# Optimization experiments

Hardware: AMD Instinct MI355X
Metric: run time of the kernel (lower is better)

The kernel has to match this reference:

```python
import jax, jax.numpy as jnp
import numpy as np
from jax import lax

K = 8  # number of KNN neighbors (excluding self)


def setup_inputs() -> dict:
    key = jax.random.key(0)
    k1, k2, k3 = jax.random.split(key, 3)
    B, H, W, C = 32, 14, 14, 2048
    OUT = 512
    x = jax.random.normal(k1, (B, H, W, C), dtype=jnp.float32)
    W1 = jax.random.normal(k2, (C, OUT), dtype=jnp.float32) * (1.0 / np.sqrt(C))
    b1 = jnp.zeros((OUT,), dtype=jnp.float32)
    W2 = jax.random.normal(k3, (OUT, OUT), dtype=jnp.float32) * (1.0 / np.sqrt(OUT))
    b2 = jnp.zeros((OUT,), dtype=jnp.float32)
    return {"x": x, "W1": W1, "b1": b1, "W2": W2, "b2": b2}


def _knn_edges(xf, k):
    # full pairwise squared-euclidean distance (monotone in cdist p=2)
    sq = jnp.sum(xf * xf, axis=-1)                      # [N]
    d2 = sq[:, None] + sq[None, :] - 2.0 * (xf @ xf.T)  # [N, N]
    _, idx = lax.top_k(-d2, k + 1)                      # smallest k+1
    knn = idx[:, 1:]                                    # drop self
    N = xf.shape[0]
    src = jnp.repeat(jnp.arange(N), k)
    dst = knn.reshape(-1)
    # GCNConv adds self-loops
    loops = jnp.arange(N)
    src = jnp.concatenate([src, loops])
    dst = jnp.concatenate([dst, loops])
    return src, dst


def _gcn_conv(h, W, b, src, dst, N):
    # PyG GCNConv: sym-normalized aggregation with self-loops
    deg = jax.ops.segment_sum(jnp.ones_like(dst, dtype=h.dtype), dst, num_segments=N)
    dinv = lax.rsqrt(jnp.maximum(deg, 1.0))
    norm = dinv[src] * dinv[dst]                        # [E]
    hw = h @ W                                          # [N, F]
    msg = hw[src] * norm[:, None]                       # gather + scale
    out = jax.ops.segment_sum(msg, dst, num_segments=N) # scatter-add
    return out + b


def reference(x, W1, b1, W2, b2):
    B, H, Wd, C = x.shape
    N = B * H * Wd
    xf = x.reshape(N, C)
    src, dst = _knn_edges(xf, K)
    h = jax.nn.relu(_gcn_conv(xf, W1, b1, src, dst, N))
    # dropout is identity in eval mode
    h = jax.nn.relu(_gcn_conv(h, W2, b2, src, dst, N))
    return h.reshape(B, H, Wd, W2.shape[1])
```

## Files before the change

### kernel.cpp

```cpp
#include <hip/hip_runtime.h>

typedef __attribute__((ext_vector_type(8))) _Float16 half8;
typedef __attribute__((ext_vector_type(4))) _Float16 half4;
typedef __attribute__((ext_vector_type(4))) float f32x4;

#define N_NODES 6272
#define CDIM    2048
#define ODIM    512
#define NPAN    49
#define NSLOT   392
#define GRID_G  1232
#define GATE    0.6f

#define XHI_OFF    0ul
#define CANDV_OFF  25690112ul
#define CANDI_OFF  35524608ul
#define SQ_OFF     40441856ul
#define KNN_OFF    40466944ul
#define DEG_OFF    41470464ul
#define DINV_OFF   41520640ul
#define RPTR_OFF   41545728ul
#define COL_OFF    41571072ul
#define W1T_OFF    41796864ul
#define W2T_OFF    43894016ul
#define HW_OFF     CANDV_OFF
#define H1H_OFF    44418304ul

__device__ __forceinline__ void gld_lds16(const void* g, void* l) {
    __builtin_amdgcn_global_load_lds(
        (const __attribute__((address_space(1))) void*)g,
        (__attribute__((address_space(3))) void*)l, 16, 0, 0);
}

__device__ __forceinline__ half8 frag_read(const char* base, int row, int s, int lane) {
    int b = (s * 4 + (lane >> 4)) ^ (row & 7);
    return *(const half8*)(base + row * 128 + b * 16);
}

#define MF(a, b, c) __builtin_amdgcn_mfma_f32_16x16x32_f16(a, b, c, 0, 0, 0)

__global__ __launch_bounds__(256) void prep_kernel(const float* __restrict__ x,
        _Float16* __restrict__ xhi, float* __restrict__ sq,
        const float* __restrict__ W1, _Float16* __restrict__ w1t,
        const float* __restrict__ W2, _Float16* __restrict__ w2t) {
    __shared__ float tile[64][65];
    int bid = blockIdx.x, tid = threadIdx.x;
    if (bid < 1568) {
        int i = bid * 4 + (tid >> 6);
        int t = tid & 63;
        const float* row = x + (size_t)i * CDIM;
        _Float16* hrow = xhi + (size_t)i * CDIM;
        float s = 0.f;
#pragma unroll
        for (int k = 0; k < 8; k++) {
            float4 v = *(const float4*)(row + (k * 64 + t) * 4);
            half4 h;
            h[0] = (_Float16)v.x; h[1] = (_Float16)v.y;
            h[2] = (_Float16)v.z; h[3] = (_Float16)v.w;
            *(half4*)(hrow + (k * 64 + t) * 4) = h;
            s += v.x * v.x + v.y * v.y + v.z * v.z + v.w * v.w;
        }
#pragma unroll
        for (int off = 32; off; off >>= 1) s += __shfl_down(s, off, 64);
        if (t == 0) sq[i] = s;
        return;
    }
    const float* W; _Float16* Wt; int K, N, idx;
    if (bid < 1824) { idx = bid - 1568; W = W1; Wt = w1t; K = CDIM; N = ODIM; }
    else            { idx = bid - 1824; W = W2; Wt = w2t; K = ODIM; N = ODIM; }
    int nkb = K / 64;
    int kb = (idx % nkb) * 64, nb = (idx / nkb) * 64;
    int r = tid >> 2, c0 = (tid & 3) * 16;
#pragma unroll
    for (int u = 0; u < 4; u++) {
        float4 v = *(const float4*)(W + (size_t)(kb + r) * N + nb + c0 + u * 4);
        tile[r][c0 + u * 4 + 0] = v.x; tile[r][c0 + u * 4 + 1] = v.y;
        tile[r][c0 + u * 4 + 2] = v.z; tile[r][c0 + u * 4 + 3] = v.w;
    }
    __syncthreads();
    int rn = tid >> 2, ck0 = (tid & 3) * 16;
#pragma unroll
    for (int u = 0; u < 4; u++) {
        half4 o;
#pragma unroll
        for (int j = 0; j < 4; j++) o[j] = (_Float16)tile[ck0 + u * 4 + j][rn];
        *(half4*)(Wt + (size_t)(nb + rn) * K + kb + ck0 + u * 4) = o;
    }
}

__global__ __launch_bounds__(256, 4) void gram_screen(
        const _Float16* __restrict__ xhi, const float* __restrict__ sq,
        float* __restrict__ candv, unsigned short* __restrict__ candi) {
    __shared__ char lds[32768];
    float* S = (float*)lds;
    float* topv = (float*)(lds + 16896);
    unsigned short* topi = (unsigned short*)(lds + 21504);
#define TOPV(r, k) topv[(r) * 9 + (k)]
#define TOPI(r, k) topi[(r) * 10 + (k)]

    int tid = threadIdx.x, lane = tid & 63, wave = tid >> 6;
    int wr = wave >> 1, wc = wave & 1;
    int l15 = lane & 15, kg = lane >> 4;

    int xcd = blockIdx.x & 7, loc = blockIdx.x >> 3;
    if (xcd != 0 && loc >= 153) return;
    int raster = (xcd == 0) ? loc : (154 + (xcd - 1) * 153 + loc);
    int t = (int)((sqrtf(8.f * (float)raster + 1.f) - 1.f) * 0.5f);
    while ((t + 1) * (t + 2) / 2 <= raster) t++;
    while (t * (t + 1) / 2 > raster) t--;
    int p = raster - t * (t + 1) / 2;
    size_t i0 = (size_t)p * 128, j0 = (size_t)t * 128;

    f32x4 acc[4][4] = {};

    int r_in = lane >> 3;
    int kb = (lane & 7) ^ r_in;
    int kadd = (kb < 4) ? kb * 8 : 1024 + (kb - 4) * 8;

#pragma unroll 1
    for (int c = 0; c < 32; c++) {
        int kk = c * 32;
#pragma unroll
        for (int g = 0; g < 8; g++) {
            int sg = wave * 8 + g;
            int tI = sg >> 4, seg = sg & 15;
            size_t row = (tI ? j0 : i0) + (size_t)(seg * 8 + r_in);
            gld_lds16(xhi + row * CDIM + kk + kadd, lds + tI * 16384 + seg * 1024);
        }
        __syncthreads();
#pragma unroll
        for (int s = 0; s < 2; s++) {
            half8 a4[4];
#pragma unroll
            for (int m = 0; m < 4; m++)
                a4[m] = frag_read(lds, wr * 64 + m * 16 + l15, s, lane);
#pragma unroll
            for (int n = 0; n < 4; n++) {
                half8 b = frag_read(lds + 16384, wc * 64 + n * 16 + l15, s, lane);
#pragma unroll
                for (int m = 0; m < 4; m++) acc[m][n] = MF(a4[m], b, acc[m][n]);
            }
        }
        __syncthreads();
    }

    float sqi[4][4];
#pragma unroll
    for (int m = 0; m < 4; m++)
#pragma unroll
        for (int r = 0; r < 4; r++)
            sqi[m][r] = sq[(int)i0 + wr * 64 + m * 16 + kg * 4 + r];
    float sqj[4];
#pragma unroll
    for (int n = 0; n < 4; n++)
        sqj[n] = sq[(int)j0 + wc * 64 + n * 16 + l15];

    if (tid < 128) {
#pragma unroll
        for (int k = 0; k < 8; k++) { TOPV(tid, k) = 3.4e38f; TOPI(tid, k) = 0xFFFF; }
    }

#pragma unroll
    for (int cs = 0; cs < 4; cs++) {
        __syncthreads();
        if (wc == (cs >> 1)) {
            const int n0 = (cs & 1) * 2;
#pragma unroll
            for (int m = 0; m < 4; m++)
#pragma unroll
                for (int nn = 0; nn < 2; nn++)
#pragma unroll
                    for (int r = 0; r < 4; r++) {
                        int row = wr * 64 + m * 16 + kg * 4 + r;
                        float d2 = sqi[m][r] + sqj[n0 + nn] - 2.f * acc[m][n0 + nn][r];
                        S[row * 33 + nn * 16 + l15] = d2;
                    }
        }
        __syncthreads();
        if (tid < 128) {
            int r = tid, gi = (int)i0 + r;
            int cbase = (int)j0 + cs * 32;
#pragma unroll 4
            for (int jj = 0; jj < 32; jj++) {
                int gj = cbase + jj;
                if (gj == gi) continue;
                float v = S[r * 33 + jj];
                float wv = TOPV(r, 7); int wi = TOPI(r, 7);
                if (v < wv || (v == wv && gj < wi)) {
                    int pos = 7;
                    while (pos > 0) {
                        float pv = TOPV(r, pos - 1); int pi = TOPI(r, pos - 1);
                        if (v < pv || (v == pv && gj < pi)) {
                            TOPV(r, pos) = pv; TOPI(r, pos) = (unsigned short)pi; pos--;
                        } else break;
                    }
                    TOPV(r, pos) = v; TOPI(r, pos) = (unsigned short)gj;
                }
            }
        }
    }
    __syncthreads();
    if (tid < 128) {
        int gi = (int)i0 + tid;
#pragma unroll
        for (int k = 0; k < 8; k++) {
            candv[(size_t)gi * NSLOT + t * 8 + k] = TOPV(tid, k);
            candi[(size_t)gi * NSLOT + t * 8 + k] = TOPI(tid, k);
        }
#pragma unroll
        for (int k = 0; k < 8; k++) { TOPV(tid, k) = 3.4e38f; TOPI(tid, k) = 0xFFFF; }
    }

    if (p < t) {
#pragma unroll
        for (int ss = 0; ss < 4; ss++) {
            __syncthreads();
            if (wr == (ss >> 1)) {
                const int mb = (ss & 1) * 2;
#pragma unroll
                for (int mm = 0; mm < 2; mm++)
#pragma unroll
                    for (int n = 0; n < 4; n++)
#pragma unroll
                        for (int r = 0; r < 4; r++) {
                            int rl  = mm * 16 + kg * 4 + r;
                            int col = wc * 64 + n * 16 + l15;
                            float d2 = sqi[mb + mm][r] + sqj[n] - 2.f * acc[mb + mm][n][r];
                            S[col * 33 + rl] = d2;
                        }
            }
            __syncthreads();
            if (tid < 128) {
                int cc = tid;
                int rbase = (int)i0 + ss * 32;
#pragma unroll 4
                for (int jj = 0; jj < 32; jj++) {
                    int gi = rbase + jj;
                    float v = S[cc * 33 + jj];
                    float wv = TOPV(cc, 7); int wi = TOPI(cc, 7);
                    if (v < wv || (v == wv && gi < wi)) {
                        int pos = 7;
                        while (pos > 0) {
                            float pv = TOPV(cc, pos - 1); int pi = TOPI(cc, pos - 1);
                            if (v < pv || (v == pv && gi < pi)) {
                                TOPV(cc, pos) = pv; TOPI(cc, pos) = (unsigned short)pi; pos--;
                            } else break;
                        }
                        TOPV(cc, pos) = v; TOPI(cc, pos) = (unsigned short)gi;
                    }
                }
            }
        }
        __syncthreads();
        if (tid < 128) {
            int gj = (int)j0 + tid;
#pragma unroll
            for (int k = 0; k < 8; k++) {
                candv[(size_t)gj * NSLOT + p * 8 + k] = TOPV(tid, k);
                candi[(size_t)gj * NSLOT + p * 8 + k] = TOPI(tid, k);
            }
        }
    }
#undef TOPV
#undef TOPI
}

__global__ __launch_bounds__(256) void knn_select_kernel(
        const float* __restrict__ candv, const unsigned short* __restrict__ candi,
        const float* __restrict__ x, const float* __restrict__ sq,
        int* __restrict__ knn) {
    int node = blockIdx.x * 4 + (threadIdx.x >> 6);
    int lane = threadIdx.x & 63;
    const float* cv = candv + (size_t)node * NSLOT;
    const unsigned short* ci = candi + (size_t)node * NSLOT;
    float v[7]; int ix[7];
#pragma unroll
    for (int u = 0; u < 7; u++) {
        int s = u * 64 + lane;
        bool ok = (s < NSLOT);
        v[u]  = ok ? cv[s] : 3.4e38f;
        ix[u] = ok ? (int)ci[s] : 0x7fffffff;
    }
    float myv16 = 3.4e38f; int myc = 0x7fffffff;
#pragma unroll 1
    for (int k = 0; k < 16; k++) {
        float bv = v[0]; int bi = ix[0];
#pragma unroll
        for (int u = 1; u < 7; u++)
            if (v[u] < bv || (v[u] == bv && ix[u] < bi)) { bv = v[u]; bi = ix[u]; }
#pragma unroll
        for (int off = 32; off; off >>= 1) {
            float ov = __shfl_xor(bv, off, 64);
            int   oi = __shfl_xor(bi, off, 64);
            if (ov < bv || (ov == bv && oi < bi)) { bv = ov; bi = oi; }
        }
        if (lane == k) { myv16 = bv; myc = bi; }
#pragma unroll
        for (int u = 0; u < 7; u++)
            if (ix[u] == bi) { v[u] = 3.4e38f; ix[u] = 0x7fffffff; }
    }
    float g7 = __shfl(myv16, 7, 64), g8 = __shfl(myv16, 8, 64);
    if (g8 - g7 > GATE) {
        if (lane < 8) knn[(size_t)node * 8 + lane] = myc;
        return;
    }
    const float* xi = x + (size_t)node * CDIM;
    float4 a[8];
#pragma unroll
    for (int g = 0; g < 8; g++) a[g] = *(const float4*)(xi + (g * 64 + lane) * 4);
    float sqi = sq[node];
    float rv = 3.4e38f; int ri = 0x7fffffff;
#pragma unroll 1
    for (int c = 0; c < 16; c++) {
        int j = __shfl(myc, c, 64);
        const float* xj = x + (size_t)j * CDIM;
        float s = 0.f;
#pragma unroll
        for (int g = 0; g < 8; g++) {
            float4 b = *(const float4*)(xj + (g * 64 + lane) * 4);
            s = fmaf(a[g].x, b.x, s); s = fmaf(a[g].y, b.y, s);
            s = fmaf(a[g].z, b.z, s); s = fmaf(a[g].w, b.w, s);
        }
#pragma unroll
        for (int off = 32; off; off >>= 1) s += __shfl_down(s, off, 64);
        float d2 = sqi + sq[j] - 2.f * s;
        d2 = __shfl(d2, 0, 64);
        if (lane == c) { rv = d2; ri = j; }
    }
#pragma unroll 1
    for (int k = 0; k < 8; k++) {
        float bv = rv; int bi = ri;
#pragma unroll
        for (int off = 8; off; off >>= 1) {
            float ov = __shfl_xor(bv, off, 64);
            int   oi = __shfl_xor(bi, off, 64);
            if (ov < bv || (ov == bv && oi < bi)) { bv = ov; bi = oi; }
        }
        bv = __shfl(bv, lane & 15, 64); bi = __shfl(bi, lane & 15, 64);
        if (lane == 0) knn[(size_t)node * 8 + k] = bi;
        if (ri == bi) { rv = 3.4e38f; ri = 0x7fffffff; }
    }
}

__global__ __launch_bounds__(1024) void graph_build_kernel(
        const int* __restrict__ knn, float* __restrict__ dinv,
        int* __restrict__ row_ptr, int* __restrict__ col) {
    __shared__ int deg_l[N_NODES];
    __shared__ int cnt_l[N_NODES];
    __shared__ int rp_l[N_NODES];
    __shared__ int partial[1024];
    int tid = threadIdx.x;
    for (int i = tid; i < N_NODES; i += 1024) { deg_l[i] = 1; cnt_l[i] = 0; }
    __syncthreads();
    for (int e = tid; e < N_NODES * 8; e += 1024) atomicAdd(&deg_l[knn[e]], 1);
    __syncthreads();
    const int CH = 7;
    int start = tid * CH;
    int end = start + CH; if (end > N_NODES) end = N_NODES;
    int s = 0;
    for (int i = start; i < end; i++) s += deg_l[i];
    partial[tid] = s;
    __syncthreads();
    if (tid == 0) {
        int run = 0;
        for (int k = 0; k < 1024; k++) { int vv = partial[k]; partial[k] = run; run += vv; }
        row_ptr[N_NODES] = run;
    }
    __syncthreads();
    int run = partial[tid];
    for (int i = start; i < end; i++) {
        rp_l[i] = run; row_ptr[i] = run;
        dinv[i] = rsqrtf((float)deg_l[i]);
        run += deg_l[i];
    }
    __syncthreads();
    for (int i = tid; i < N_NODES; i += 1024) {
        int p0 = rp_l[i] + atomicAdd(&cnt_l[i], 1);
        col[p0] = i;
#pragma unroll
        for (int j = 0; j < 8; j++) {
            int d = knn[i * 8 + j];
            int q = rp_l[d] + atomicAdd(&cnt_l[d], 1);
            col[q] = i;
        }
    }
}

__global__ __launch_bounds__(256) void hgemm_nt_kernel(
        const _Float16* __restrict__ A, const _Float16* __restrict__ Bt,
        float* __restrict__ C, int M, int N, int K) {
    __shared__ char Alds[16384], Blds[16384];
    int tid = threadIdx.x, lane = tid & 63, wave = tid >> 6;
    int wr = wave >> 1, wc = wave & 1;
    int l15 = lane & 15, kg = lane >> 4;
    int nt = N >> 7;
    int i0 = (blockIdx.x / nt) * 128, j0 = (blockIdx.x % nt) * 128;
    f32x4 acc[4][4] = {};

#pragma unroll 1
    for (int kk = 0; kk < K; kk += 64) {
        __syncthreads();
#pragma unroll
        for (int g = 0; g < 4; g++) {
            int R = wave * 32 + g * 8;
            int swzk = ((lane & 7) ^ (lane >> 3)) << 3;
            const _Float16* ga = A + (size_t)(i0 + R + (lane >> 3)) * K + kk + swzk;
            gld_lds16(ga, Alds + R * 128);
            const _Float16* gb = Bt + (size_t)(j0 + R + (lane >> 3)) * K + kk + swzk;
            gld_lds16(gb, Blds + R * 128);
        }
        __syncthreads();
#pragma unroll
        for (int s = 0; s < 2; s++) {
            half8 a[4], b[4];
#pragma unroll
            for (int m = 0; m < 4; m++) a[m] = frag_read(Alds, wr * 64 + m * 16 + l15, s, lane);
#pragma unroll
            for (int n = 0; n < 4; n++) b[n] = frag_read(Blds, wc * 64 + n * 16 + l15, s, lane);
#pragma unroll
            for (int m = 0; m < 4; m++)
#pragma unroll
                for (int n = 0; n < 4; n++)
                    acc[m][n] = __builtin_amdgcn_mfma_f32_16x16x32_f16(a[m], b[n], acc[m][n], 0, 0, 0);
        }
    }
#pragma unroll
    for (int m = 0; m < 4; m++)
#pragma unroll
        for (int n = 0; n < 4; n++)
#pragma unroll
            for (int r = 0; r < 4; r++) {
                int row = i0 + wr * 64 + m * 16 + kg * 4 + r;
                int colj = j0 + wc * 64 + n * 16 + l15;
                C[(size_t)row * N + colj] = acc[m][n][r];
            }
}

template <bool HALF>
__global__ __launch_bounds__(256) void aggregate_kernel(
        const float* __restrict__ hw, const int* __restrict__ row_ptr,
        const int* __restrict__ col, const float* __restrict__ dinv,
        const float* __restrict__ bias, void* __restrict__ outp) {
    int node = blockIdx.x * 4 + (threadIdx.x >> 6);
    int lane = threadIdx.x & 63;
    int e0 = row_ptr[node], e1 = row_ptr[node + 1];
    float4 acc0 = {0.f, 0.f, 0.f, 0.f}, acc1 = {0.f, 0.f, 0.f, 0.f};
    for (int e = e0; e < e1; e++) {
        int s = col[e];
        float w = dinv[s];
        const float* hr = hw + (size_t)s * ODIM;
        float4 v0 = *(const float4*)(hr + lane * 4);
        float4 v1 = *(const float4*)(hr + 256 + lane * 4);
        acc0.x = fmaf(w, v0.x, acc0.x); acc0.y = fmaf(w, v0.y, acc0.y);
        acc0.z = fmaf(w, v0.z, acc0.z); acc0.w = fmaf(w, v0.w, acc0.w);
        acc1.x = fmaf(w, v1.x, acc1.x); acc1.y = fmaf(w, v1.y, acc1.y);
        acc1.z = fmaf(w, v1.z, acc1.z); acc1.w = fmaf(w, v1.w, acc1.w);
    }
    float wd = dinv[node];
    float4 b0 = *(const float4*)(bias + lane * 4);
    float4 b1 = *(const float4*)(bias + 256 + lane * 4);
    float o[8];
    o[0] = fmaxf(fmaf(acc0.x, wd, b0.x), 0.f);
    o[1] = fmaxf(fmaf(acc0.y, wd, b0.y), 0.f);
    o[2] = fmaxf(fmaf(acc0.z, wd, b0.z), 0.f);
    o[3] = fmaxf(fmaf(acc0.w, wd, b0.w), 0.f);
    o[4] = fmaxf(fmaf(acc1.x, wd, b1.x), 0.f);
    o[5] = fmaxf(fmaf(acc1.y, wd, b1.y), 0.f);
    o[6] = fmaxf(fmaf(acc1.z, wd, b1.z), 0.f);
    o[7] = fmaxf(fmaf(acc1.w, wd, b1.w), 0.f);
    if (HALF) {
        _Float16* out = (_Float16*)outp;
        half4 h0, h1;
#pragma unroll
        for (int j = 0; j < 4; j++) { h0[j] = (_Float16)o[j]; h1[j] = (_Float16)o[4 + j]; }
        *(half4*)(out + (size_t)node * ODIM + lane * 4)       = h0;
        *(half4*)(out + (size_t)node * ODIM + 256 + lane * 4) = h1;
    } else {
        float* out = (float*)outp;
        float4 f0 = {o[0], o[1], o[2], o[3]}, f1 = {o[4], o[5], o[6], o[7]};
        *(float4*)(out + (size_t)node * ODIM + lane * 4)       = f0;
        *(float4*)(out + (size_t)node * ODIM + 256 + lane * 4) = f1;
    }
}

extern "C" void kernel_launch(void* const* d_in, const int* in_sizes, int n_in,
                              void* d_out, int out_size, void* d_ws, size_t ws_size,
                              hipStream_t stream) {
    const float* x  = (const float*)d_in[0];
    const float* W1 = (const float*)d_in[1];
    const float* b1 = (const float*)d_in[2];
    const float* W2 = (const float*)d_in[3];
    const float* b2 = (const float*)d_in[4];
    float* out = (float*)d_out;
    char* ws = (char*)d_ws;

    _Float16* xhi  = (_Float16*)(ws + XHI_OFF);
    float* candv   = (float*)(ws + CANDV_OFF);
    unsigned short* candi = (unsigned short*)(ws + CANDI_OFF);
    float* sq      = (float*)(ws + SQ_OFF);
    int*   knn     = (int*)  (ws + KNN_OFF);
    float* dinv    = (float*)(ws + DINV_OFF);
    int*   row_ptr = (int*)  (ws + RPTR_OFF);
    int*   col     = (int*)  (ws + COL_OFF);
    _Float16* w1t  = (_Float16*)(ws + W1T_OFF);
    _Float16* w2t  = (_Float16*)(ws + W2T_OFF);
    float* hw      = (float*)(ws + HW_OFF);
    _Float16* h1h  = (_Float16*)(ws + H1H_OFF);

    prep_kernel<<<1888, 256, 0, stream>>>(x, xhi, sq, W1, w1t, W2, w2t);
    gram_screen<<<GRID_G, 256, 0, stream>>>(xhi, sq, candv, candi);
    knn_select_kernel<<<N_NODES / 4, 256, 0, stream>>>(candv, candi, x, sq, knn);
    graph_build_kernel<<<1, 1024, 0, stream>>>(knn, dinv, row_ptr, col);

    hgemm_nt_kernel<<<(N_NODES / 128) * (ODIM / 128), 256, 0, stream>>>(xhi, w1t, hw, N_NODES, ODIM, CDIM);
    aggregate_kernel<true><<<N_NODES / 4, 256, 0, stream>>>(hw, row_ptr, col, dinv, b1, (void*)h1h);
    hgemm_nt_kernel<<<(N_NODES / 128) * (ODIM / 128), 256, 0, stream>>>(h1h, w2t, hw, N_NODES, ODIM, ODIM);
    aggregate_kernel<false><<<N_NODES / 4, 256, 0, stream>>>(hw, row_ptr, col, dinv, b2, (void*)out);
}
```

Before: 1.181 ms.

## Store GCN GEMM output in fp16, retile hgemm to 64x128 with XCD swizzle

The feature GEMMs now write hw in fp16 instead of fp32, and the aggregation kernels gather half8 rows. This halves the bytes written by each GEMM and read by the bandwidth-bound neighbour gather. The hgemm kernel uses 64x128 tiles, one shared LDS buffer and an XCD-aware block swizzle, which doubles the block count for better occupancy and cache locality. The Gram screen now loads contiguous 64-wide K chunks instead of two split halves. The cost is fp16 rounding of the intermediate features and more blocks re-reading the B operand.

```diff
diff --git a/kernel.cpp b/kernel.cpp
--- a/kernel.cpp
+++ b/kernel.cpp
@@ -17,7 +17,6 @@
 #define CANDI_OFF  35524608ul
 #define SQ_OFF     40441856ul
 #define KNN_OFF    40466944ul
-#define DEG_OFF    41470464ul
 #define DINV_OFF   41520640ul
 #define RPTR_OFF   41545728ul
 #define COL_OFF    41571072ul
@@ -114,18 +113,17 @@
     f32x4 acc[4][4] = {};
 
     int r_in = lane >> 3;
-    int kb = (lane & 7) ^ r_in;
-    int kadd = (kb < 4) ? kb * 8 : 1024 + (kb - 4) * 8;
+    int skb = (lane & 7) ^ r_in;
 
 #pragma unroll 1
     for (int c = 0; c < 32; c++) {
-        int kk = c * 32;
+        int kk = c * 64;
 #pragma unroll
         for (int g = 0; g < 8; g++) {
             int sg = wave * 8 + g;
             int tI = sg >> 4, seg = sg & 15;
             size_t row = (tI ? j0 : i0) + (size_t)(seg * 8 + r_in);
-            gld_lds16(xhi + row * CDIM + kk + kadd, lds + tI * 16384 + seg * 1024);
+            gld_lds16(xhi + row * CDIM + kk + skb * 8, lds + tI * 16384 + seg * 1024);
         }
         __syncthreads();
 #pragma unroll
@@ -388,98 +386,99 @@
 
 __global__ __launch_bounds__(256) void hgemm_nt_kernel(
         const _Float16* __restrict__ A, const _Float16* __restrict__ Bt,
-        float* __restrict__ C, int M, int N, int K) {
-    __shared__ char Alds[16384], Blds[16384];
+        _Float16* __restrict__ C, int M, int N, int K) {
+    __shared__ char lds[24576];
     int tid = threadIdx.x, lane = tid & 63, wave = tid >> 6;
-    int wr = wave >> 1, wc = wave & 1;
     int l15 = lane & 15, kg = lane >> 4;
     int nt = N >> 7;
-    int i0 = (blockIdx.x / nt) * 128, j0 = (blockIdx.x % nt) * 128;
-    f32x4 acc[4][4] = {};
+    int nblk = (M >> 6) * nt;
+    int per = nblk >> 3;
+    int swz = (blockIdx.x & 7) * per + (blockIdx.x >> 3);
+    int i0 = (swz % (M >> 6)) * 64, j0 = (swz / (M >> 6)) * 128;
+    f32x4 acc[4][2] = {};
+
+    int r_in = lane >> 3;
+    int skb = (lane & 7) ^ r_in;
 
 #pragma unroll 1
     for (int kk = 0; kk < K; kk += 64) {
         __syncthreads();
 #pragma unroll
-        for (int g = 0; g < 4; g++) {
-            int R = wave * 32 + g * 8;
-            int swzk = ((lane & 7) ^ (lane >> 3)) << 3;
-            const _Float16* ga = A + (size_t)(i0 + R + (lane >> 3)) * K + kk + swzk;
-            gld_lds16(ga, Alds + R * 128);
-            const _Float16* gb = Bt + (size_t)(j0 + R + (lane >> 3)) * K + kk + swzk;
-            gld_lds16(gb, Blds + R * 128);
+        for (int g = 0; g < 6; g++) {
+            int sg = wave * 6 + g;
+            if (sg < 8) {
+                gld_lds16(A + (size_t)(i0 + sg * 8 + r_in) * K + kk + skb * 8,
+                          lds + sg * 1024);
+            } else {
+                int seg = sg - 8;
+                gld_lds16(Bt + (size_t)(j0 + seg * 8 + r_in) * K + kk + skb * 8,
+                          lds + 8192 + seg * 1024);
+            }
         }
         __syncthreads();
 #pragma unroll
         for (int s = 0; s < 2; s++) {
-            half8 a[4], b[4];
-#pragma unroll
-            for (int m = 0; m < 4; m++) a[m] = frag_read(Alds, wr * 64 + m * 16 + l15, s, lane);
-#pragma unroll
-            for (int n = 0; n < 4; n++) b[n] = frag_read(Blds, wc * 64 + n * 16 + l15, s, lane);
-#pragma unroll
-            for (int m = 0; m < 4; m++)
-#pragma unroll
-                for (int n = 0; n < 4; n++)
-                    acc[m][n] = __builtin_amdgcn_mfma_f32_16x16x32_f16(a[m], b[n], acc[m][n], 0, 0, 0);
+            half8 a[4];
+#pragma unroll
+            for (int m = 0; m < 4; m++) a[m] = frag_read(lds, m * 16 + l15, s, lane);
+#pragma unroll
+            for (int n = 0; n < 2; n++) {
+                half8 b = frag_read(lds + 8192, wave * 32 + n * 16 + l15, s, lane);
+#pragma unroll
+                for (int m = 0; m < 4; m++) acc[m][n] = MF(a[m], b, acc[m][n]);
+            }
         }
     }
 #pragma unroll
     for (int m = 0; m < 4; m++)
 #pragma unroll
-        for (int n = 0; n < 4; n++)
+        for (int n = 0; n < 2; n++)
 #pragma unroll
             for (int r = 0; r < 4; r++) {
-                int row = i0 + wr * 64 + m * 16 + kg * 4 + r;
-                int colj = j0 + wc * 64 + n * 16 + l15;
-                C[(size_t)row * N + colj] = acc[m][n][r];
-            }
-}
-
-template <bool HALF>
+                int row = i0 + m * 16 + kg * 4 + r;
+                int colj = j0 + wave * 32 + n * 16 + l15;
+                C[(size_t)row * N + colj] = (_Float16)acc[m][n][r];
+            }
+}
+
+template <bool HALF_OUT>
 __global__ __launch_bounds__(256) void aggregate_kernel(
-        const float* __restrict__ hw, const int* __restrict__ row_ptr,
+        const _Float16* __restrict__ hw, const int* __restrict__ row_ptr,
         const int* __restrict__ col, const float* __restrict__ dinv,
         const float* __restrict__ bias, void* __restrict__ outp) {
     int node = blockIdx.x * 4 + (threadIdx.x >> 6);
     int lane = threadIdx.x & 63;
     int e0 = row_ptr[node], e1 = row_ptr[node + 1];
-    float4 acc0 = {0.f, 0.f, 0.f, 0.f}, acc1 = {0.f, 0.f, 0.f, 0.f};
+    float acc[8] = {};
     for (int e = e0; e < e1; e++) {
         int s = col[e];
         float w = dinv[s];
-        const float* hr = hw + (size_t)s * ODIM;
-        float4 v0 = *(const float4*)(hr + lane * 4);
-        float4 v1 = *(const float4*)(hr + 256 + lane * 4);
-        acc0.x = fmaf(w, v0.x, acc0.x); acc0.y = fmaf(w, v0.y, acc0.y);
-        acc0.z = fmaf(w, v0.z, acc0.z); acc0.w = fmaf(w, v0.w, acc0.w);
-        acc1.x = fmaf(w, v1.x, acc1.x); acc1.y = fmaf(w, v1.y, acc1.y);
-        acc1.z = fmaf(w, v1.z, acc1.z); acc1.w = fmaf(w, v1.w, acc1.w);
+        half8 v = *(const half8*)(hw + (size_t)s * ODIM + lane * 8);
+#pragma unroll
+        for (int j = 0; j < 8; j++) acc[j] = fmaf(w, (float)v[j], acc[j]);
     }
     float wd = dinv[node];
-    float4 b0 = *(const float4*)(bias + lane * 4);
-    float4 b1 = *(const float4*)(bias + 256 + lane * 4);
+    float4 b0 = *(const float4*)(bias + lane * 8);
+    float4 b1 = *(const float4*)(bias + lane * 8 + 4);
     float o[8];
-    o[0] = fmaxf(fmaf(acc0.x, wd, b0.x), 0.f);
-    o[1] = fmaxf(fmaf(acc0.y, wd, b0.y), 0.f);
-    o[2] = fmaxf(fmaf(acc0.z, wd, b0.z), 0.f);
-    o[3] = fmaxf(fmaf(acc0.w, wd, b0.w), 0.f);
-    o[4] = fmaxf(fmaf(acc1.x, wd, b1.x), 0.f);
-    o[5] = fmaxf(fmaf(acc1.y, wd, b1.y), 0.f);
-    o[6] = fmaxf(fmaf(acc1.z, wd, b1.z), 0.f);
-    o[7] = fmaxf(fmaf(acc1.w, wd, b1.w), 0.f);
-    if (HALF) {
-        _Float16* out = (_Float16*)outp;
-        half4 h0, h1;
-#pragma unroll
-        for (int j = 0; j < 4; j++) { h0[j] = (_Float16)o[j]; h1[j] = (_Float16)o[4 + j]; }
-        *(half4*)(out + (size_t)node * ODIM + lane * 4)       = h0;
-        *(half4*)(out + (size_t)node * ODIM + 256 + lane * 4) = h1;
+    o[0] = fmaxf(fmaf(acc[0], wd, b0.x), 0.f);
+    o[1] = fmaxf(fmaf(acc[1], wd, b0.y), 0.f);
+    o[2] = fmaxf(fmaf(acc[2], wd, b0.z), 0.f);
+    o[3] = fmaxf(fmaf(acc[3], wd, b0.w), 0.f);
+    o[4] = fmaxf(fmaf(acc[4], wd, b1.x), 0.f);
+    o[5] = fmaxf(fmaf(acc[5], wd, b1.y), 0.f);
+    o[6] = fmaxf(fmaf(acc[6], wd, b1.z), 0.f);
+    o[7] = fmaxf(fmaf(acc[7], wd, b1.w), 0.f);
+    if (HALF_OUT) {
+        half8 h;
+#pragma unroll
+        for (int j = 0; j < 8; j++) h[j] = (_Float16)o[j];
+        *(half8*)((_Float16*)outp + (size_t)node * ODIM + lane * 8) = h;
     } else {
         float* out = (float*)outp;
         float4 f0 = {o[0], o[1], o[2], o[3]}, f1 = {o[4], o[5], o[6], o[7]};
-        *(float4*)(out + (size_t)node * ODIM + lane * 4)       = f0;
-        *(float4*)(out + (size_t)node * ODIM + 256 + lane * 4) = f1;
+        *(float4*)(out + (size_t)node * ODIM + lane * 8)     = f0;
+        *(float4*)(out + (size_t)node * ODIM + lane * 8 + 4) = f1;
     }
 }
 
@@ -504,7 +503,7 @@
     int*   col     = (int*)  (ws + COL_OFF);
     _Float16* w1t  = (_Float16*)(ws + W1T_OFF);
     _Float16* w2t  = (_Float16*)(ws + W2T_OFF);
-    float* hw      = (float*)(ws + HW_OFF);
+    _Float16* hw   = (_Float16*)(ws + HW_OFF);
     _Float16* h1h  = (_Float16*)(ws + H1H_OFF);
 
     prep_kernel<<<1888, 256, 0, stream>>>(x, xhi, sq, W1, w1t, W2, w2t);
@@ -512,8 +511,8 @@
     knn_select_kernel<<<N_NODES / 4, 256, 0, stream>>>(candv, candi, x, sq, knn);
     graph_build_kernel<<<1, 1024, 0, stream>>>(knn, dinv, row_ptr, col);
 
-    hgemm_nt_kernel<<<(N_NODES / 128) * (ODIM / 128), 256, 0, stream>>>(xhi, w1t, hw, N_NODES, ODIM, CDIM);
+    hgemm_nt_kernel<<<(N_NODES / 64) * (ODIM / 128), 256, 0, stream>>>(xhi, w1t, hw, N_NODES, ODIM, CDIM);
     aggregate_kernel<true><<<N_NODES / 4, 256, 0, stream>>>(hw, row_ptr, col, dinv, b1, (void*)h1h);
-    hgemm_nt_kernel<<<(N_NODES / 128) * (ODIM / 128), 256, 0, stream>>>(h1h, w2t, hw, N_NODES, ODIM, ODIM);
+    hgemm_nt_kernel<<<(N_NODES / 64) * (ODIM / 128), 256, 0, stream>>>(h1h, w2t, hw, N_NODES, ODIM, ODIM);
     aggregate_kernel<false><<<N_NODES / 4, 256, 0, stream>>>(hw, row_ptr, col, dinv, b2, (void*)out);
 }
```

Measured after the change: 1.131 ms. 1.04x faster.
